# Optimization experiments

Measured on AMD Instinct MI355X. Metric: run time of the kernel, lower is better.

The kernel has to match this reference:

```python
import jax, jax.numpy as jnp
import numpy as np
import math

B, S, D_MODEL = 2, 2048, 1024
NUM_HEADS, D_KEY, D_VALUE = 16, 64, 64


def setup_inputs() -> dict:
    key = jax.random.key(0)
    ks = jax.random.split(key, 7)
    query = jax.random.normal(ks[0], (B, S, D_MODEL), dtype=jnp.float32)
    k_in = jax.random.normal(ks[1], (B, S, D_MODEL), dtype=jnp.float32)
    v_in = jax.random.normal(ks[2], (B, S, D_MODEL), dtype=jnp.float32)
    # boolean mask, True = masked out (masked_fill_ semantics); causal mask
    mask = jnp.triu(jnp.ones((S, S), dtype=bool), k=1)[None, None, :, :]
    scale = 1.0 / math.sqrt(D_MODEL)
    w_q = jax.random.normal(ks[3], (D_MODEL, NUM_HEADS * D_KEY), dtype=jnp.float32) * scale
    w_k = jax.random.normal(ks[4], (D_MODEL, NUM_HEADS * D_KEY), dtype=jnp.float32) * scale
    w_v = jax.random.normal(ks[5], (D_MODEL, NUM_HEADS * D_VALUE), dtype=jnp.float32) * scale
    w_o = jax.random.normal(ks[6], (NUM_HEADS * D_VALUE, D_MODEL), dtype=jnp.float32) * scale
    return {"query": query, "key": k_in, "value": v_in, "mask": mask,
            "w_q": w_q, "w_k": w_k, "w_v": w_v, "w_o": w_o}


def reference(query, key, value, mask, w_q, w_k, w_v, w_o):
    b, sq, _ = query.shape
    sk = key.shape[1]
    # projections, split heads: [B, H, S, d]
    q = (query @ w_q).reshape(b, sq, NUM_HEADS, D_KEY).transpose(0, 2, 1, 3)
    k = (key @ w_k).reshape(b, sk, NUM_HEADS, D_KEY).transpose(0, 2, 1, 3)
    v = (value @ w_v).reshape(b, sk, NUM_HEADS, D_VALUE).transpose(0, 2, 1, 3)
    # scaled scores [B, H, Sq, Sk], eager masked softmax (as in source)
    scores = jnp.einsum('bhqd,bhkd->bhqk', q, k) / math.sqrt(D_KEY)
    scores = jnp.where(mask, -jnp.inf, scores)
    attn = jax.nn.softmax(scores, axis=-1)
    # AV, merge heads, output projection (dropout is identity in eval / p=0)
    out = jnp.einsum('bhqk,bhkd->bhqd', attn, v)
    out = out.transpose(0, 2, 1, 3).reshape(b, sq, NUM_HEADS * D_VALUE)
    return out @ w_o
```

## Files before the change

kernel.cpp:

```cpp
#include <hip/hip_runtime.h>


typedef __attribute__((ext_vector_type(8))) short v8s;
typedef __attribute__((ext_vector_type(4))) float v4f;

#define MFMA16(a, b, c) __builtin_amdgcn_mfma_f32_16x16x32_bf16(a, b, c, 0, 0, 0)

#define GLOBAL_AS __attribute__((address_space(1)))
#define LDS_AS __attribute__((address_space(3)))

__device__ __forceinline__ void gload_lds16(const void* g, void* l) {
  __builtin_amdgcn_global_load_lds((const GLOBAL_AS void*)g, (LDS_AS void*)l, 16, 0, 0);
}

__device__ __forceinline__ short f2bf(float f) {
  union { float f; unsigned u; } x; x.f = f;
  unsigned r = x.u + 0x7fffu + ((x.u >> 16) & 1u);
  return (short)(r >> 16);
}

__device__ __forceinline__ unsigned cvtpk_bf16(float a, float b) {
  unsigned r;
  asm("v_cvt_pk_bf16_f32 %0, %1, %2" : "=v"(r) : "v"(a), "v"(b));
  return r;
}

__device__ __forceinline__ float exp2_hw(float x) {
  float r;
  asm("v_exp_f32 %0, %1" : "=v"(r) : "v"(x));
  return r;
}

__global__ __launch_bounds__(256) void wtrans_kernel(const float* __restrict__ w0,
                                                     const float* __restrict__ w1,
                                                     const float* __restrict__ w2,
                                                     const float* __restrict__ w3,
                                                     short* __restrict__ wtbase) {
  __shared__ __align__(16) short tile[64 * 72];
  const int NN = 1024;
  int z = blockIdx.z;
  const float* W = (z == 0) ? w0 : (z == 1) ? w1 : (z == 2) ? w2 : w3;
  short* Wt = wtbase + ((z < 3) ? ((size_t)(z + 1) << 20) : 0);
  float scale = (z == 0) ? 0.125f * 1.44269504f : 1.0f;
  int n0 = blockIdx.x * 64, k0 = blockIdx.y * 64;
  int t = threadIdx.x;
  int r = t >> 4;
  int c4 = (t & 15) * 4;
  for (int rr = r; rr < 64; rr += 16) {
    float4 f = *(const float4*)(W + (size_t)(k0 + rr) * NN + n0 + c4);
    tile[(c4 + 0) * 72 + rr] = f2bf(f.x * scale);
    tile[(c4 + 1) * 72 + rr] = f2bf(f.y * scale);
    tile[(c4 + 2) * 72 + rr] = f2bf(f.z * scale);
    tile[(c4 + 3) * 72 + rr] = f2bf(f.w * scale);
  }
  __syncthreads();
  int nr = t >> 2, kc = (t & 3) * 16;
  v8s v0 = *(const v8s*)&tile[nr * 72 + kc];
  v8s v1 = *(const v8s*)&tile[nr * 72 + kc + 8];
  *(v8s*)(Wt + (size_t)(n0 + nr) * NN + k0 + kc) = v0;
  *(v8s*)(Wt + (size_t)(n0 + nr) * NN + k0 + kc + 8) = v1;
}

__global__ __launch_bounds__(256) void vtrans_kernel(const short* __restrict__ Vb,
                                                     short* __restrict__ Vtg) {
  __shared__ __align__(16) short T[64 * 72];
  const int S = 2048, DM = 1024;
  int s0 = blockIdx.x * 64;
  int bh = blockIdx.y;
  int b = bh >> 4, h = bh & 15;
  int t = threadIdx.x;
  int srow = t >> 2, sc = (t & 3) * 16;
  const short* src = Vb + (size_t)(b * S + s0 + srow) * DM + h * 64 + sc;
  v8s a = *(const v8s*)src;
  v8s c = *(const v8s*)(src + 8);
#pragma unroll
  for (int j = 0; j < 8; ++j) {
    int jj = (j + srow) & 7;
    T[(sc + jj) * 72 + srow] = a[jj];
  }
#pragma unroll
  for (int j = 0; j < 8; ++j) {
    int jj = (j + srow) & 7;
    T[(sc + 8 + jj) * 72 + srow] = c[jj];
  }
  __syncthreads();
  int dr = t >> 2, oc = (t & 3) * 16;
  short* dst = Vtg + (size_t)bh * 64 * S + (size_t)dr * S + s0 + oc;
  *(v8s*)dst = *(const v8s*)&T[dr * 72 + oc];
  *(v8s*)(dst + 8) = *(const v8s*)&T[dr * 72 + oc + 8];
}

template <bool A_F32, bool OUT_F32>
__global__ __launch_bounds__(256) void gemm2_kernel(
    const float* __restrict__ a0, const float* __restrict__ a1,
    const float* __restrict__ a2,
    const short* __restrict__ Ab, size_t sA,
    const short* __restrict__ Btb, size_t sB,
    short* __restrict__ Cb, float* __restrict__ Cf, size_t sC,
    int M, int N, int K) {
  __shared__ __align__(16) short As[2][128 * 32];
  __shared__ __align__(16) short Bs[2][128 * 32];

  int gx = gridDim.x, gy = gridDim.y;
  int id = blockIdx.x + gx * (blockIdx.y + gy * blockIdx.z);
  int nwg = gx * gy * gridDim.z;
  int v = (id & 7) * (nwg >> 3) + (id >> 3);
  int bx = v % gx;
  int by = (v / gx) % gy;
  int bz = v / (gx * gy);

  const short* Bt = Btb + (size_t)bz * sB;
  int row0 = by * 128, col0 = bx * 128;
  int t = threadIdx.x, lane = t & 63, w = t >> 6;
  int wm = (w >> 1) * 64, wn = (w & 1) * 64;
  int lr = lane & 15, lg = lane >> 4;

  v4f acc[4][4];
#pragma unroll
  for (int i = 0; i < 4; ++i)
#pragma unroll
    for (int j = 0; j < 4; ++j) acc[i][j] = {0.f, 0.f, 0.f, 0.f};

  int rl = lane >> 2, sl = lane & 3;
  int scol = ((sl ^ (rl ^ (rl >> 2))) & 3) * 8;
  const short* gB = Bt + (size_t)(col0 + w * 16 + rl) * K + scol;
  const short* gA_s =
      A_F32 ? nullptr
            : (Ab + (size_t)bz * sA + (size_t)(row0 + w * 16 + rl) * K + scol);
  const size_t rstep = (size_t)64 * K;

  int ar = t >> 1, kh = t & 1;
  int sar = (ar ^ (ar >> 2)) & 3;
  int ps0 = ((2 * kh) ^ sar) * 8;
  int ps1 = ((2 * kh + 1) ^ sar) * 8;
  const float* gA_f = nullptr;
  if (A_F32) {
    const float* Af = (bz == 0) ? a0 : (bz == 1) ? a1 : a2;
    gA_f = Af + (size_t)(row0 + ar) * K + kh * 16;
  }
  float4 fa[4];

#define STAGE_B(buf, k0_)                                   \
  {                                                         \
    gload_lds16(gB + (k0_), &Bs[buf][w * 512]);             \
    gload_lds16(gB + rstep + (k0_), &Bs[buf][(w + 4) * 512]); \
  }
#define STAGE_A_DMA(buf, k0_)                               \
  {                                                         \
    gload_lds16(gA_s + (k0_), &As[buf][w * 512]);           \
    gload_lds16(gA_s + rstep + (k0_), &As[buf][(w + 4) * 512]); \
  }
#define STAGE_A_LOAD(k0_)                                   \
  {                                                         \
    _Pragma("unroll") for (int j = 0; j < 4; ++j)           \
        fa[j] = *(const float4*)(gA_f + (k0_) + j * 4);     \
  }
#define STAGE_A_WRITE(buf)                                  \
  {                                                         \
    uint4 pk0, pk1;                                         \
    pk0.x = cvtpk_bf16(fa[0].x, fa[0].y);                   \
    pk0.y = cvtpk_bf16(fa[0].z, fa[0].w);                   \
    pk0.z = cvtpk_bf16(fa[1].x, fa[1].y);                   \
    pk0.w = cvtpk_bf16(fa[1].z, fa[1].w);                   \
    pk1.x = cvtpk_bf16(fa[2].x, fa[2].y);                   \
    pk1.y = cvtpk_bf16(fa[2].z, fa[2].w);                   \
    pk1.z = cvtpk_bf16(fa[3].x, fa[3].y);                   \
    pk1.w = cvtpk_bf16(fa[3].z, fa[3].w);                   \
    *(uint4*)&As[buf][ar * 32 + ps0] = pk0;                 \
    *(uint4*)&As[buf][ar * 32 + ps1] = pk1;                 \
  }

  if (A_F32) {
    STAGE_A_LOAD(0);
    STAGE_B(0, 0);
    STAGE_A_WRITE(0);
  } else {
    STAGE_B(0, 0);
    STAGE_A_DMA(0, 0);
  }
  __syncthreads();

  int cur = 0;
  int rsw = (lr ^ (lr >> 2)) & 3;
  for (int k0 = 0; k0 < K; k0 += 32) {
    bool next = (k0 + 32 < K);
    if (next) {
      if (A_F32) STAGE_A_LOAD(k0 + 32);
      STAGE_B(cur ^ 1, k0 + 32);
      if (!A_F32) STAGE_A_DMA(cur ^ 1, k0 + 32);
    }
    v8s af[4], bg[4];
#pragma unroll
    for (int mf = 0; mf < 4; ++mf)
      af[mf] = *(const v8s*)&As[cur][(wm + mf * 16 + lr) * 32 + ((lg ^ rsw) * 8)];
#pragma unroll
    for (int nf = 0; nf < 4; ++nf)
      bg[nf] = *(const v8s*)&Bs[cur][(wn + nf * 16 + lr) * 32 + ((lg ^ rsw) * 8)];
    __builtin_amdgcn_s_setprio(1);
#pragma unroll
    for (int mf = 0; mf < 4; ++mf)
#pragma unroll
      for (int nf = 0; nf < 4; ++nf)
        acc[mf][nf] = MFMA16(af[mf], bg[nf], acc[mf][nf]);
    __builtin_amdgcn_s_setprio(0);
    if (next && A_F32) STAGE_A_WRITE(cur ^ 1);
    __syncthreads();
    cur ^= 1;
  }
#undef STAGE_B
#undef STAGE_A_DMA
#undef STAGE_A_LOAD
#undef STAGE_A_WRITE

#pragma unroll
  for (int mf = 0; mf < 4; ++mf)
#pragma unroll
    for (int nf = 0; nf < 4; ++nf)
#pragma unroll
      for (int r = 0; r < 4; ++r) {
        int row = row0 + wm + mf * 16 + lg * 4 + r;
        int col = col0 + wn + nf * 16 + lr;
        if (OUT_F32)
          (Cf + (size_t)bz * sC)[(size_t)row * N + col] = acc[mf][nf][r];
        else
          (Cb + (size_t)bz * sC)[(size_t)row * N + col] = f2bf(acc[mf][nf][r]);
      }
}

__global__ __launch_bounds__(512, 4) void attn_kernel(const short* __restrict__ Qm,
                                                      const short* __restrict__ Km,
                                                      const short* __restrict__ Vt_g,
                                                      short* __restrict__ Cm) {
  const int S = 2048, DM = 1024;
  __shared__ __align__(16) short lds[21504];
  short* Ks0 = lds;
  short* Vs0 = lds + 8192;
  short* Pt = lds + 16384;
  v4f* scr = (v4f*)lds;

  int id = blockIdx.y * 16 + blockIdx.x;
  int v = (id & 7) * 64 + (id >> 3);
  int bh = v >> 4;
  int px = v & 15;
  int b = bh >> 4, h = bh & 15;
  int t = threadIdx.x, lane = t & 63, w = t >> 6;
  int g = w & 3, hh = w >> 2;
  int lr = lane & 15, lg = lane >> 4;
  size_t base = (size_t)b * S * DM + h * 64;
  size_t vbase = (size_t)bh * 64 * S;

  int srow = w * 8 + (lane >> 3);
  int scol = ((lane & 7) ^ (lane >> 3)) * 8;
  const short* gK = Km + base + (size_t)srow * DM + scol;
  const short* gV = Vt_g + vbase + (size_t)srow * S + scol;
  int sw = (lr & 7) * 8;

  const v8s vone = {0x3F80, 0x3F80, 0x3F80, 0x3F80,
                    0x3F80, 0x3F80, 0x3F80, 0x3F80};

#define ATTN_STAGE(buf, kt_)                                                  \
  do {                                                                        \
    size_t k0_ = (size_t)(kt_) * 64;                                          \
    gload_lds16(gK + k0_ * DM, &Ks0[(buf) * 4096 + w * 512]);                 \
    gload_lds16(gV + k0_, &Vs0[(buf) * 4096 + w * 512]);                      \
  } while (0)

  short* Cp = Cm + base;

#pragma unroll 1
  for (int qsel = 0; qsel < 2; ++qsel) {
    int qt = qsel ? px : (31 - px);
    int qbase = qt * 64 + g * 16;
    int qg = qbase + lr;
    int nkt = qt + 1;

    const short* Qp = Qm + base + (size_t)(qbase + lr) * DM + lg * 8;
    v8s q0 = *(const v8s*)Qp;
    v8s q1 = *(const v8s*)(Qp + 32);

    v4f o[5];
#pragma unroll
    for (int d4 = 0; d4 < 5; ++d4) o[d4] = {0.f, 0.f, 0.f, 0.f};

    ATTN_STAGE(0, 0);
    __syncthreads();
    int cur = 0;
#pragma unroll 1
    for (int kt = 0; kt < nkt; ++kt) {
      if (kt + 1 < nkt) ATTN_STAGE(cur ^ 1, kt + 1);
      int k0 = kt * 64;
      const short* Kc = &Ks0[cur * 4096];
      const short* Vc = &Vs0[cur * 4096];

      v8s ka0[2], ka1[2], vf[4];
#pragma unroll
      for (int t2 = 0; t2 < 2; ++t2) {
        int kr = hh * 32 + t2 * 16 + lr;
        ka0[t2] = *(const v8s*)&Kc[kr * 64 + ((lg * 8) ^ sw)];
        ka1[t2] = *(const v8s*)&Kc[kr * 64 + ((32 + lg * 8) ^ sw)];
      }
#pragma unroll
      for (int d4 = 0; d4 < 4; ++d4)
        vf[d4] = *(const v8s*)&Vc[(d4 * 16 + lr) * 64 + ((hh * 32 + lg * 8) ^ sw)];

      v4f st[2];
      __builtin_amdgcn_s_setprio(1);
#pragma unroll
      for (int t2 = 0; t2 < 2; ++t2) {
        v4f s = {0.f, 0.f, 0.f, 0.f};
        s = MFMA16(ka0[t2], q0, s);
        s = MFMA16(ka1[t2], q1, s);
        st[t2] = s;
      }
      __builtin_amdgcn_s_setprio(0);

      if (kt == nkt - 1) {
#pragma unroll
        for (int t2 = 0; t2 < 2; ++t2)
#pragma unroll
          for (int r = 0; r < 4; ++r)
            if (k0 + hh * 32 + t2 * 16 + lg * 4 + r > qg) st[t2][r] = -1e30f;
      }

#pragma unroll
      for (int t2 = 0; t2 < 2; ++t2) {
        uint2 u;
        u.x = cvtpk_bf16(exp2_hw(st[t2][0]), exp2_hw(st[t2][1]));
        u.y = cvtpk_bf16(exp2_hw(st[t2][2]), exp2_hw(st[t2][3]));
        *(uint2*)&Pt[w * 640 + lr * 40 + t2 * 16 + lg * 4] = u;
      }
      v8s pa = *(const v8s*)&Pt[w * 640 + lr * 40 + lg * 8];

      __builtin_amdgcn_s_setprio(1);
#pragma unroll
      for (int d4 = 0; d4 < 4; ++d4) o[d4] = MFMA16(pa, vf[d4], o[d4]);
      o[4] = MFMA16(pa, vone, o[4]);
      __builtin_amdgcn_s_setprio(0);
      __syncthreads();
      cur ^= 1;
    }

    if (hh == 1) {
#pragma unroll
      for (int d4 = 0; d4 < 5; ++d4) scr[(g * 5 + d4) * 64 + lane] = o[d4];
    }
    __syncthreads();
    if (hh == 0) {
#pragma unroll
      for (int d4 = 0; d4 < 5; ++d4) {
        v4f p = scr[(g * 5 + d4) * 64 + lane];
#pragma unroll
        for (int r = 0; r < 4; ++r) o[d4][r] += p[r];
      }
      float sv[4];
#pragma unroll
      for (int r = 0; r < 4; ++r) sv[r] = 1.0f / o[4][r];
#pragma unroll
      for (int r = 0; r < 4; ++r)
#pragma unroll
        for (int d4 = 0; d4 < 4; ++d4)
          Cp[(size_t)(qbase + lg * 4 + r) * DM + d4 * 16 + lr] =
              f2bf(o[d4][r] * sv[r]);
    }
    __syncthreads();
  }
#undef ATTN_STAGE
}

extern "C" void kernel_launch(void* const* d_in, const int* in_sizes, int n_in,
                              void* d_out, int out_size, void* d_ws, size_t ws_size,
                              hipStream_t stream) {
  const float* q_in = (const float*)d_in[0];
  const float* k_in = (const float*)d_in[1];
  const float* v_in = (const float*)d_in[2];
  const float* w_q = (const float*)d_in[4];
  const float* w_k = (const float*)d_in[5];
  const float* w_v = (const float*)d_in[6];
  const float* w_o = (const float*)d_in[7];
  float* outp = (float*)d_out;

  short* ws = (short*)d_ws;
  const size_t M1 = (size_t)1 << 20;
  short* Wto = ws;
  short* Wtq = ws + 1 * M1;
  short* Qb = ws + 4 * M1;
  short* Kb = ws + 8 * M1;
  short* Vb = ws + 12 * M1;
  short* Vtg = ws + 16 * M1;
  short* Cb = Vb;
  dim3 tb(256);
  dim3 tba(512);

  wtrans_kernel<<<dim3(16, 16, 4), tb, 0, stream>>>(w_q, w_k, w_v, w_o, ws);
  gemm2_kernel<true, false><<<dim3(8, 32, 3), tb, 0, stream>>>(
      q_in, k_in, v_in, nullptr, 0, Wtq, M1, Qb, nullptr, 4 * M1,
      4096, 1024, 1024);
  vtrans_kernel<<<dim3(32, 32), tb, 0, stream>>>(Vb, Vtg);
  attn_kernel<<<dim3(16, 32), tba, 0, stream>>>(Qb, Kb, Vtg, Cb);
  gemm2_kernel<false, true><<<dim3(8, 32, 1), tb, 0, stream>>>(
      nullptr, nullptr, nullptr, Cb, 0, Wto, 0, nullptr, outp, 0,
      4096, 1024, 1024);
}
```

Baseline: 115.0 us.

## Fuse V transpose into projection GEMM epilogue and double-register A prefetch

Removes the separate V transpose kernel by having the V slice of the QKV projection GEMM write its output directly in the transposed [bh, d, s] layout. This saves one launch and one full read and write of V through global memory. The fp32 A-operand path is also unrolled by two with two register buffers, so global loads are issued two steps ahead. In exchange, the transposed epilogue makes narrower 8-byte strided stores, and the extra register buffer raises register pressure.

```diff
diff --git a/kernel.cpp b/kernel.cpp
--- a/kernel.cpp
+++ b/kernel.cpp
@@ -61,42 +61,14 @@
   *(v8s*)(Wt + (size_t)(n0 + nr) * NN + k0 + kc + 8) = v1;
 }
 
-__global__ __launch_bounds__(256) void vtrans_kernel(const short* __restrict__ Vb,
-                                                     short* __restrict__ Vtg) {
-  __shared__ __align__(16) short T[64 * 72];
-  const int S = 2048, DM = 1024;
-  int s0 = blockIdx.x * 64;
-  int bh = blockIdx.y;
-  int b = bh >> 4, h = bh & 15;
-  int t = threadIdx.x;
-  int srow = t >> 2, sc = (t & 3) * 16;
-  const short* src = Vb + (size_t)(b * S + s0 + srow) * DM + h * 64 + sc;
-  v8s a = *(const v8s*)src;
-  v8s c = *(const v8s*)(src + 8);
-#pragma unroll
-  for (int j = 0; j < 8; ++j) {
-    int jj = (j + srow) & 7;
-    T[(sc + jj) * 72 + srow] = a[jj];
-  }
-#pragma unroll
-  for (int j = 0; j < 8; ++j) {
-    int jj = (j + srow) & 7;
-    T[(sc + 8 + jj) * 72 + srow] = c[jj];
-  }
-  __syncthreads();
-  int dr = t >> 2, oc = (t & 3) * 16;
-  short* dst = Vtg + (size_t)bh * 64 * S + (size_t)dr * S + s0 + oc;
-  *(v8s*)dst = *(const v8s*)&T[dr * 72 + oc];
-  *(v8s*)(dst + 8) = *(const v8s*)&T[dr * 72 + oc + 8];
-}
-
-template <bool A_F32, bool OUT_F32>
+template <bool A_F32, bool OUT_F32, bool V_TRANS>
 __global__ __launch_bounds__(256) void gemm2_kernel(
     const float* __restrict__ a0, const float* __restrict__ a1,
     const float* __restrict__ a2,
     const short* __restrict__ Ab, size_t sA,
     const short* __restrict__ Btb, size_t sB,
     short* __restrict__ Cb, float* __restrict__ Cf, size_t sC,
+    short* __restrict__ Vt,
     int M, int N, int K) {
   __shared__ __align__(16) short As[2][128 * 32];
   __shared__ __align__(16) short Bs[2][128 * 32];
@@ -138,7 +110,7 @@
     const float* Af = (bz == 0) ? a0 : (bz == 1) ? a1 : a2;
     gA_f = Af + (size_t)(row0 + ar) * K + kh * 16;
   }
-  float4 fa[4];
+  float4 faA[4], faB[4];
 
 #define STAGE_B(buf, k0_)                                   \
   {                                                         \
@@ -150,81 +122,113 @@
     gload_lds16(gA_s + (k0_), &As[buf][w * 512]);           \
     gload_lds16(gA_s + rstep + (k0_), &As[buf][(w + 4) * 512]); \
   }
-#define STAGE_A_LOAD(k0_)                                   \
+#define STAGE_A_LOAD(dst, k0_)                              \
   {                                                         \
     _Pragma("unroll") for (int j = 0; j < 4; ++j)           \
-        fa[j] = *(const float4*)(gA_f + (k0_) + j * 4);     \
-  }
-#define STAGE_A_WRITE(buf)                                  \
+        dst[j] = *(const float4*)(gA_f + (k0_) + j * 4);    \
+  }
+#define STAGE_A_WRITE(buf, src)                             \
   {                                                         \
     uint4 pk0, pk1;                                         \
-    pk0.x = cvtpk_bf16(fa[0].x, fa[0].y);                   \
-    pk0.y = cvtpk_bf16(fa[0].z, fa[0].w);                   \
-    pk0.z = cvtpk_bf16(fa[1].x, fa[1].y);                   \
-    pk0.w = cvtpk_bf16(fa[1].z, fa[1].w);                   \
-    pk1.x = cvtpk_bf16(fa[2].x, fa[2].y);                   \
-    pk1.y = cvtpk_bf16(fa[2].z, fa[2].w);                   \
-    pk1.z = cvtpk_bf16(fa[3].x, fa[3].y);                   \
-    pk1.w = cvtpk_bf16(fa[3].z, fa[3].w);                   \
+    pk0.x = cvtpk_bf16(src[0].x, src[0].y);                 \
+    pk0.y = cvtpk_bf16(src[0].z, src[0].w);                 \
+    pk0.z = cvtpk_bf16(src[1].x, src[1].y);                 \
+    pk0.w = cvtpk_bf16(src[1].z, src[1].w);                 \
+    pk1.x = cvtpk_bf16(src[2].x, src[2].y);                 \
+    pk1.y = cvtpk_bf16(src[2].z, src[2].w);                 \
+    pk1.z = cvtpk_bf16(src[3].x, src[3].y);                 \
+    pk1.w = cvtpk_bf16(src[3].z, src[3].w);                 \
     *(uint4*)&As[buf][ar * 32 + ps0] = pk0;                 \
     *(uint4*)&As[buf][ar * 32 + ps1] = pk1;                 \
   }
+#define COMPUTE(buf)                                                          \
+  {                                                                           \
+    v8s af[4], bg[4];                                                         \
+    _Pragma("unroll") for (int mf = 0; mf < 4; ++mf)                          \
+        af[mf] = *(const v8s*)&As[buf][(wm + mf * 16 + lr) * 32 +             \
+                                       ((lg ^ rsw) * 8)];                     \
+    _Pragma("unroll") for (int nf = 0; nf < 4; ++nf)                          \
+        bg[nf] = *(const v8s*)&Bs[buf][(wn + nf * 16 + lr) * 32 +             \
+                                       ((lg ^ rsw) * 8)];                     \
+    __builtin_amdgcn_s_setprio(1);                                            \
+    _Pragma("unroll") for (int mf = 0; mf < 4; ++mf)                          \
+        _Pragma("unroll") for (int nf = 0; nf < 4; ++nf)                      \
+            acc[mf][nf] = MFMA16(af[mf], bg[nf], acc[mf][nf]);                \
+    __builtin_amdgcn_s_setprio(0);                                            \
+  }
+
+  int rsw = (lr ^ (lr >> 2)) & 3;
+  int cur = 0;
 
   if (A_F32) {
-    STAGE_A_LOAD(0);
+    STAGE_A_LOAD(faA, 0);
     STAGE_B(0, 0);
-    STAGE_A_WRITE(0);
+    STAGE_A_WRITE(0, faA);
+    STAGE_A_LOAD(faB, 32);
+    __syncthreads();
+    for (int k0 = 0; k0 < K; k0 += 64) {
+      if (k0 + 64 < K) STAGE_A_LOAD(faA, k0 + 64);
+      if (k0 + 32 < K) STAGE_B(cur ^ 1, k0 + 32);
+      COMPUTE(cur);
+      if (k0 + 32 < K) STAGE_A_WRITE(cur ^ 1, faB);
+      __syncthreads();
+      cur ^= 1;
+      if (k0 + 96 < K) STAGE_A_LOAD(faB, k0 + 96);
+      if (k0 + 64 < K) STAGE_B(cur ^ 1, k0 + 64);
+      COMPUTE(cur);
+      if (k0 + 64 < K) STAGE_A_WRITE(cur ^ 1, faA);
+      __syncthreads();
+      cur ^= 1;
+    }
   } else {
     STAGE_B(0, 0);
     STAGE_A_DMA(0, 0);
-  }
-  __syncthreads();
-
-  int cur = 0;
-  int rsw = (lr ^ (lr >> 2)) & 3;
-  for (int k0 = 0; k0 < K; k0 += 32) {
-    bool next = (k0 + 32 < K);
-    if (next) {
-      if (A_F32) STAGE_A_LOAD(k0 + 32);
-      STAGE_B(cur ^ 1, k0 + 32);
-      if (!A_F32) STAGE_A_DMA(cur ^ 1, k0 + 32);
+    __syncthreads();
+    for (int k0 = 0; k0 < K; k0 += 32) {
+      if (k0 + 32 < K) {
+        STAGE_B(cur ^ 1, k0 + 32);
+        STAGE_A_DMA(cur ^ 1, k0 + 32);
+      }
+      COMPUTE(cur);
+      __syncthreads();
+      cur ^= 1;
     }
-    v8s af[4], bg[4];
-#pragma unroll
-    for (int mf = 0; mf < 4; ++mf)
-      af[mf] = *(const v8s*)&As[cur][(wm + mf * 16 + lr) * 32 + ((lg ^ rsw) * 8)];
-#pragma unroll
-    for (int nf = 0; nf < 4; ++nf)
-      bg[nf] = *(const v8s*)&Bs[cur][(wn + nf * 16 + lr) * 32 + ((lg ^ rsw) * 8)];
-    __builtin_amdgcn_s_setprio(1);
-#pragma unroll
-    for (int mf = 0; mf < 4; ++mf)
-#pragma unroll
-      for (int nf = 0; nf < 4; ++nf)
-        acc[mf][nf] = MFMA16(af[mf], bg[nf], acc[mf][nf]);
-    __builtin_amdgcn_s_setprio(0);
-    if (next && A_F32) STAGE_A_WRITE(cur ^ 1);
-    __syncthreads();
-    cur ^= 1;
   }
 #undef STAGE_B
 #undef STAGE_A_DMA
 #undef STAGE_A_LOAD
 #undef STAGE_A_WRITE
-
-#pragma unroll
-  for (int mf = 0; mf < 4; ++mf)
-#pragma unroll
-    for (int nf = 0; nf < 4; ++nf)
-#pragma unroll
-      for (int r = 0; r < 4; ++r) {
-        int row = row0 + wm + mf * 16 + lg * 4 + r;
+#undef COMPUTE
+
+  if (V_TRANS && bz == 2) {
+#pragma unroll
+    for (int mf = 0; mf < 4; ++mf)
+#pragma unroll
+      for (int nf = 0; nf < 4; ++nf) {
         int col = col0 + wn + nf * 16 + lr;
-        if (OUT_F32)
-          (Cf + (size_t)bz * sC)[(size_t)row * N + col] = acc[mf][nf][r];
-        else
-          (Cb + (size_t)bz * sC)[(size_t)row * N + col] = f2bf(acc[mf][nf][r]);
-      }
+        int row = row0 + wm + mf * 16 + lg * 4;
+        int bh = ((row >> 11) << 4) + (col >> 6);
+        int d = col & 63, s = row & 2047;
+        uint2 u;
+        u.x = cvtpk_bf16(acc[mf][nf][0], acc[mf][nf][1]);
+        u.y = cvtpk_bf16(acc[mf][nf][2], acc[mf][nf][3]);
+        *(uint2*)&Vt[((size_t)bh * 64 + d) * 2048 + s] = u;
+      }
+  } else {
+#pragma unroll
+    for (int mf = 0; mf < 4; ++mf)
+#pragma unroll
+      for (int nf = 0; nf < 4; ++nf)
+#pragma unroll
+        for (int r = 0; r < 4; ++r) {
+          int row = row0 + wm + mf * 16 + lg * 4 + r;
+          int col = col0 + wn + nf * 16 + lr;
+          if (OUT_F32)
+            (Cf + (size_t)bz * sC)[(size_t)row * N + col] = acc[mf][nf][r];
+          else
+            (Cb + (size_t)bz * sC)[(size_t)row * N + col] = f2bf(acc[mf][nf][r]);
+        }
+  }
 }
 
 __global__ __launch_bounds__(512, 4) void attn_kernel(const short* __restrict__ Qm,
@@ -385,19 +389,17 @@
   short* Wtq = ws + 1 * M1;
   short* Qb = ws + 4 * M1;
   short* Kb = ws + 8 * M1;
-  short* Vb = ws + 12 * M1;
-  short* Vtg = ws + 16 * M1;
-  short* Cb = Vb;
+  short* Vtg = ws + 12 * M1;
+  short* Cb = ws + 16 * M1;
   dim3 tb(256);
   dim3 tba(512);
 
   wtrans_kernel<<<dim3(16, 16, 4), tb, 0, stream>>>(w_q, w_k, w_v, w_o, ws);
-  gemm2_kernel<true, false><<<dim3(8, 32, 3), tb, 0, stream>>>(
-      q_in, k_in, v_in, nullptr, 0, Wtq, M1, Qb, nullptr, 4 * M1,
+  gemm2_kernel<true, false, true><<<dim3(8, 32, 3), tb, 0, stream>>>(
+      q_in, k_in, v_in, nullptr, 0, Wtq, M1, Qb, nullptr, 4 * M1, Vtg,
       4096, 1024, 1024);
-  vtrans_kernel<<<dim3(32, 32), tb, 0, stream>>>(Vb, Vtg);
   attn_kernel<<<dim3(16, 32), tba, 0, stream>>>(Qb, Kb, Vtg, Cb);
-  gemm2_kernel<false, true><<<dim3(8, 32, 1), tb, 0, stream>>>(
-      nullptr, nullptr, nullptr, Cb, 0, Wto, 0, nullptr, outp, 0,
+  gemm2_kernel<false, true, false><<<dim3(8, 32, 1), tb, 0, stream>>>(
+      nullptr, nullptr, nullptr, Cb, 0, Wto, 0, nullptr, outp, 0, nullptr,
       4096, 1024, 1024);
 }
```

Measured after the change: 121.4 us. +5.6%, slower.
